# Performance work log

Hardware: AMD Instinct MI355X
Metric: run time of the kernel (lower is better)

## Reference

```python
import jax, jax.numpy as jnp
import numpy as np

B, N, R = 4, 16, 64        # batch, permuted axis size, inner spatial size
M, S = N // 2, R * 2       # block count, block size


def _glorot(key, shape):
    fan_in, fan_out = shape[-2], shape[-1]
    lim = np.sqrt(6.0 / (fan_in + fan_out)).astype(np.float32)
    return jax.random.uniform(key, shape, jnp.float32, -lim, lim)


def setup_inputs() -> dict:
    key = jax.random.key(0)
    ks = jax.random.split(key, 10)
    inp = {
        "x": jax.random.normal(ks[0], (B, N, R, N, R, 2), jnp.float32),
        "perm_idx": jax.random.permutation(ks[1], N).astype(jnp.int32),
    }
    for i, name in enumerate(["hr1", "hi1", "hr2", "hi2", "hr3", "hi3", "hr4", "hi4"]):
        inp[name] = _glorot(ks[2 + i], (M, S, S))
    return inp


def _bilin(v, p_right, p_left):
    # v: (B, m, s, m, s). First contract the last s-axis against p_right's
    # block matmuls (block index = axis 3), then the axis-2 s-axis against
    # p_left's block matmuls (block index = axis 1).
    t = jnp.einsum('bmiaj,ajk->bmiak', v, p_right)
    return jnp.einsum('xbjci,bjk->xbkci', t, p_left)


def reference(x, perm_idx, hr1, hi1, hr2, hi2, hr3, hi3, hr4, hi4):
    m = x.shape[1] // 2
    s = x.shape[2] * 2
    n, r = m * 2, s // 2
    x = x.take(perm_idx, axis=1).take(perm_idx, axis=3)
    x = x.reshape((-1, m, s, m, s, 2))
    x_re, x_im = x[..., 0], x[..., 1]

    y_re = (_bilin(x_re, hr1, hr1) + _bilin(x_re, hi1, hi1)
            + _bilin(x_im, hi2, hr2) + _bilin(x_im, hr2, hi2))
    y_im = (_bilin(x_im, hr3, hr3) + _bilin(x_im, hi3, hi3)
            + _bilin(x_re, hi4, hr4) + _bilin(x_re, hr4, hi4))

    y = jnp.stack([y_re, y_im], axis=-1)
    return y.reshape((-1, n, r, n, r, 2))
```

## Files before the change

kernel.cpp:

```cpp
#include <hip/hip_runtime.h>
#include <hip/hip_bf16.h>
#include <stdint.h>

typedef __attribute__((ext_vector_type(8))) short bf16x8;
typedef __attribute__((ext_vector_type(4))) float f32x4;
typedef __attribute__((ext_vector_type(16))) float f32x16;

#define MFMA32(a, b, c) __builtin_amdgcn_mfma_f32_32x32x16_bf16((a), (b), (c), 0, 0, 0)

__device__ __forceinline__ unsigned short f2bf_rn(float f) {
    union { __bf16 b; unsigned short u; } v;
    v.b = (__bf16)f;
    return v.u;
}

__device__ __forceinline__ unsigned int pk2(float lo, float hi) {
    union { unsigned short s[2]; unsigned int u; } r;
    r.s[0] = f2bf_rn(lo); r.s[1] = f2bf_rn(hi);
    return r.u;
}

__device__ __forceinline__ void gload_lds16(const void* g, void* l) {
    __builtin_amdgcn_global_load_lds(
        (const __attribute__((address_space(1))) void*)g,
        (__attribute__((address_space(3))) void*)l, 16, 0, 0);
}

__global__ __launch_bounds__(256) void prep_h(
    const float* __restrict__ h0, const float* __restrict__ h1,
    const float* __restrict__ h2, const float* __restrict__ h3,
    const float* __restrict__ h4, const float* __restrict__ h5,
    const float* __restrict__ h6, const float* __restrict__ h7,
    unsigned short* __restrict__ ht)
{
    const float* hmap[8] = {h0, h1, h2, h3, h4, h5, h6, h7};
    const int wg = blockIdx.x;
    const int jblk = wg >> 2, qt = wg & 3;
    const float* src = hmap[jblk >> 3] + (jblk & 7) * 16384;
    unsigned short* dst = ht + jblk * 16384;
    __shared__ unsigned short tile[32 * 129];
    const int t = threadIdx.x;
    #pragma unroll
    for (int i = 0; i < 16; ++i) {
        int idx = t + 256 * i;
        int r = idx >> 5, kk = idx & 31;
        tile[kk * 129 + r] = f2bf_rn(src[r * 128 + qt * 32 + kk]);
    }
    __syncthreads();
    #pragma unroll
    for (int i = 0; i < 16; ++i) {
        int idx = t + 256 * i;
        int k = idx >> 7, r = idx & 127;
        dst[(qt * 32 + k) * 128 + r] = tile[k * 129 + r];
    }
}

__global__ __launch_bounds__(256, 1) void bilin_main(
    const float* __restrict__ x, const int* __restrict__ perm,
    const unsigned short* __restrict__ ht, float* __restrict__ out)
{
    const int wg = blockIdx.x;
    const int q = wg & 7, p = (wg >> 3) & 7, b = wg >> 6;
    const int tid = threadIdx.x;
    const int lane = tid & 63, wn = tid >> 6;
    const int l31 = lane & 31, hl = lane >> 5;

    __shared__ __align__(16) unsigned short smem[81920];
    unsigned short* xre_lds = smem;
    unsigned short* xim_lds = smem + 16384;
    unsigned short* llds = smem + 65536;

    constexpr int cseq[8]  = {0, 1, 6, 7, 2, 3, 4, 5};
    constexpr int rperm[8] = {0, 1, 3, 2, 4, 5, 7, 6};

    const int wubase = tid & ~63;
    auto stage_h = [&](unsigned short* dst, int blk) {
        const unsigned short* src = ht + blk * 16384;
        #pragma unroll
        for (int r = 0; r < 8; ++r) {
            const int idx = r * 256 + tid;
            const int row = idx >> 4, cin = idx & 15;
            gload_lds16(src + row * 128 + ((cin ^ (row & 15)) << 3),
                        dst + ((r * 256 + wubase) << 3));
        }
    };

    auto ldr = [&](const unsigned short* base, int row, int ch) -> bf16x8 {
        return *(const bf16x8*)(base + row * 128 + ((ch ^ (row & 15)) << 3));
    };

    auto stage_x_both = [&]() {
        #pragma unroll
        for (int i = 0; i < 8; ++i) {
            const int idx = i * 256 + tid;
            const int row = idx >> 4, cin = idx & 15;
            const int n1 = perm[2 * p + (row >> 6)];
            const int n2 = perm[2 * q + (cin >> 3)];
            const int r1 = row & 63, r2 = (cin & 7) * 8;
            const float* sp = x + ((size_t)((b * 16 + n1) * 64 + r1) * 1024
                                   + n2 * 64 + r2) * 2;
            float4 v0 = *(const float4*)(sp);
            float4 v1 = *(const float4*)(sp + 4);
            float4 v2 = *(const float4*)(sp + 8);
            float4 v3 = *(const float4*)(sp + 12);
            bf16x8 re, im;
            re[0] = (short)f2bf_rn(v0.x); re[1] = (short)f2bf_rn(v0.z);
            re[2] = (short)f2bf_rn(v1.x); re[3] = (short)f2bf_rn(v1.z);
            re[4] = (short)f2bf_rn(v2.x); re[5] = (short)f2bf_rn(v2.z);
            re[6] = (short)f2bf_rn(v3.x); re[7] = (short)f2bf_rn(v3.z);
            im[0] = (short)f2bf_rn(v0.y); im[1] = (short)f2bf_rn(v0.w);
            im[2] = (short)f2bf_rn(v1.y); im[3] = (short)f2bf_rn(v1.w);
            im[4] = (short)f2bf_rn(v2.y); im[5] = (short)f2bf_rn(v2.w);
            im[6] = (short)f2bf_rn(v3.y); im[7] = (short)f2bf_rn(v3.w);
            const int woff = row * 128 + ((cin ^ (row & 15)) << 3);
            *(bf16x8*)(xre_lds + woff) = re;
            *(bf16x8*)(xim_lds + woff) = im;
        }
    };

    bf16x8 xf[4][8];
    auto load_xf = [&](const unsigned short* plane) {
        #pragma unroll
        for (int m2 = 0; m2 < 4; ++m2)
            #pragma unroll
            for (int ks = 0; ks < 8; ++ks)
                xf[m2][ks] = ldr(plane, m2 * 32 + l31, 2 * ks + hl);
    };

    stage_h(smem + 32768, rperm[0] * 8 + q);
    stage_h(llds, 0 * 8 + p);
    stage_x_both();
    __syncthreads();
    load_xf(xre_lds);

    f32x16 yre[4], yim[4];
    #pragma unroll
    for (int i = 0; i < 4; ++i) {
        #pragma unroll
        for (int e = 0; e < 16; ++e) { yre[i][e] = 0.f; yim[i][e] = 0.f; }
    }

    #pragma unroll
    for (int cc = 0; cc < 8; ++cc) {
        const unsigned short* wb = smem + 32768 + (cc & 1) * 16384;

        if (cc < 7)
            stage_h(smem + 32768 + ((cc + 1) & 1) * 16384,
                    rperm[cseq[cc + 1]] * 8 + q);

        if (cc == 4) load_xf(xim_lds);

        bf16x8 wfr[8];
        #pragma unroll
        for (int ks = 0; ks < 8; ++ks)
            wfr[ks] = ldr(wb, wn * 32 + l31, 2 * ks + hl);
        f32x16 u[4];
        #pragma unroll
        for (int m2 = 0; m2 < 4; ++m2)
            #pragma unroll
            for (int e = 0; e < 16; ++e) u[m2][e] = 0.f;
        #pragma unroll
        for (int ks = 0; ks < 8; ++ks)
            #pragma unroll
            for (int m2 = 0; m2 < 4; ++m2)
                u[m2] = MFMA32(xf[m2][ks], wfr[ks], u[m2]);

        __syncthreads();

        union UF { unsigned int d[4]; bf16x8 v; };
        UF ufu[8];
        #pragma unroll
        for (int t = 0; t < 8; ++t) {
            const int f = t >> 1, qa = (t & 1) * 2, qb = qa + 1;
            unsigned int lo0 = pk2(u[f][4 * qa + 0], u[f][4 * qa + 1]);
            unsigned int lo1 = pk2(u[f][4 * qa + 2], u[f][4 * qa + 3]);
            unsigned int hi0 = pk2(u[f][4 * qb + 0], u[f][4 * qb + 1]);
            unsigned int hi1 = pk2(u[f][4 * qb + 2], u[f][4 * qb + 3]);
            unsigned int send0 = hl ? lo0 : hi0;
            unsigned int send1 = hl ? lo1 : hi1;
            unsigned int sx0 = (unsigned int)__shfl_xor((int)send0, 32);
            unsigned int sx1 = (unsigned int)__shfl_xor((int)send1, 32);
            ufu[t].d[0] = hl ? sx0 : lo0;
            ufu[t].d[1] = hl ? sx1 : lo1;
            ufu[t].d[2] = hl ? hi0 : sx0;
            ufu[t].d[3] = hl ? hi1 : sx1;
        }
        const bool isRe = (cc & 3) < 2;
        bf16x8 lcur[4], lnxt[4];
        #pragma unroll
        for (int mt = 0; mt < 4; ++mt)
            lcur[mt] = ldr(llds, mt * 32 + l31, hl);
        #pragma unroll
        for (int t = 0; t < 8; ++t) {
            if (t < 7) {
                #pragma unroll
                for (int mt = 0; mt < 4; ++mt)
                    lnxt[mt] = ldr(llds, mt * 32 + l31, 2 * (t + 1) + hl);
            }
            #pragma unroll
            for (int mt = 0; mt < 4; ++mt) {
                if (isRe) yre[mt] = MFMA32(lcur[mt], ufu[t].v, yre[mt]);
                else      yim[mt] = MFMA32(lcur[mt], ufu[t].v, yim[mt]);
            }
            #pragma unroll
            for (int mt = 0; mt < 4; ++mt) lcur[mt] = lnxt[mt];
        }

        __syncthreads();
        if (cc < 7)
            stage_h(llds, cseq[cc + 1] * 8 + p);
    }

    float2* o2 = (float2*)out;
    #pragma unroll
    for (int mt = 0; mt < 4; ++mt)
        #pragma unroll
        for (int j = 0; j < 16; ++j) {
            const int row = mt * 32 + (j & 3) + 8 * (j >> 2) + 4 * hl;
            float2 v;
            v.x = yre[mt][j];
            v.y = yim[mt][j];
            o2[(size_t)(b * 1024 + p * 128 + row) * 1024
               + q * 128 + wn * 32 + l31] = v;
        }
}

extern "C" void kernel_launch(void* const* d_in, const int* in_sizes, int n_in,
                              void* d_out, int out_size, void* d_ws, size_t ws_size,
                              hipStream_t stream) {
    const float* x  = (const float*)d_in[0];
    const int* perm = (const int*)d_in[1];
    unsigned short* htp = (unsigned short*)d_ws;

    hipLaunchKernelGGL(prep_h, dim3(256), dim3(256), 0, stream,
        (const float*)d_in[2], (const float*)d_in[3], (const float*)d_in[4],
        (const float*)d_in[5], (const float*)d_in[6], (const float*)d_in[7],
        (const float*)d_in[8], (const float*)d_in[9], htp);
    hipLaunchKernelGGL(bilin_main, dim3(256), dim3(256), 0, stream,
        x, perm, htp, (float*)d_out);
}
```

Baseline: 38.19 us.

## Process real and imaginary chunks per phase; spill x imaginary plane to workspace

The eight sequential chunk iterations become four phases. Each phase computes one real-output and one imaginary-output chunk, using separate LDS buffers for the re/im right and left weight blocks, which halves the number of barrier-separated stages. To free LDS for the extra weight buffers, the imaginary x plane is written to a per-workgroup global workspace and copied back into LDS with global_load_lds while phase 0 runs. This adds global traffic and relies on the workspace being large enough and on writes from other threads in the block being visible after a barrier.

```diff
diff --git a/kernel.cpp b/kernel.cpp
--- a/kernel.cpp
+++ b/kernel.cpp
@@ -57,7 +57,9 @@
 
 __global__ __launch_bounds__(256, 1) void bilin_main(
     const float* __restrict__ x, const int* __restrict__ perm,
-    const unsigned short* __restrict__ ht, float* __restrict__ out)
+    const unsigned short* __restrict__ ht,
+    unsigned short* __restrict__ ximws,
+    float* __restrict__ out)
 {
     const int wg = blockIdx.x;
     const int q = wg & 7, p = (wg >> 3) & 7, b = wg >> 6;
@@ -66,11 +68,14 @@
     const int l31 = lane & 31, hl = lane >> 5;
 
     __shared__ __align__(16) unsigned short smem[81920];
-    unsigned short* xre_lds = smem;
-    unsigned short* xim_lds = smem + 16384;
-    unsigned short* llds = smem + 65536;
-
-    constexpr int cseq[8]  = {0, 1, 6, 7, 2, 3, 4, 5};
+    unsigned short* xplane = smem;
+    unsigned short* wre = smem + 16384;
+    unsigned short* wim = smem + 32768;
+    unsigned short* lre = smem + 49152;
+    unsigned short* lim = smem + 65536;
+
+    constexpr int pre_[4]  = {0, 1, 2, 3};
+    constexpr int pim_[4]  = {6, 7, 4, 5};
     constexpr int rperm[8] = {0, 1, 3, 2, 4, 5, 7, 6};
 
     const int wubase = tid & ~63;
@@ -88,6 +93,8 @@
     auto ldr = [&](const unsigned short* base, int row, int ch) -> bf16x8 {
         return *(const bf16x8*)(base + row * 128 + ((ch ^ (row & 15)) << 3));
     };
+
+    unsigned short* myxim = ximws + (size_t)wg * 16384;
 
     auto stage_x_both = [&]() {
         #pragma unroll
@@ -113,48 +120,34 @@
             im[4] = (short)f2bf_rn(v2.y); im[5] = (short)f2bf_rn(v2.w);
             im[6] = (short)f2bf_rn(v3.y); im[7] = (short)f2bf_rn(v3.w);
             const int woff = row * 128 + ((cin ^ (row & 15)) << 3);
-            *(bf16x8*)(xre_lds + woff) = re;
-            *(bf16x8*)(xim_lds + woff) = im;
+            *(bf16x8*)(xplane + woff) = re;
+            *(bf16x8*)(myxim + woff) = im;
+        }
+    };
+
+    auto restage_xim = [&]() {
+        #pragma unroll
+        for (int r = 0; r < 8; ++r) {
+            const int idx = r * 256 + tid;
+            gload_lds16(myxim + ((size_t)idx << 3),
+                        xplane + ((r * 256 + wubase) << 3));
         }
     };
 
     bf16x8 xf[4][8];
-    auto load_xf = [&](const unsigned short* plane) {
+    auto load_xf = [&]() {
         #pragma unroll
         for (int m2 = 0; m2 < 4; ++m2)
             #pragma unroll
             for (int ks = 0; ks < 8; ++ks)
-                xf[m2][ks] = ldr(plane, m2 * 32 + l31, 2 * ks + hl);
-    };
-
-    stage_h(smem + 32768, rperm[0] * 8 + q);
-    stage_h(llds, 0 * 8 + p);
-    stage_x_both();
-    __syncthreads();
-    load_xf(xre_lds);
-
-    f32x16 yre[4], yim[4];
-    #pragma unroll
-    for (int i = 0; i < 4; ++i) {
-        #pragma unroll
-        for (int e = 0; e < 16; ++e) { yre[i][e] = 0.f; yim[i][e] = 0.f; }
-    }
-
-    #pragma unroll
-    for (int cc = 0; cc < 8; ++cc) {
-        const unsigned short* wb = smem + 32768 + (cc & 1) * 16384;
-
-        if (cc < 7)
-            stage_h(smem + 32768 + ((cc + 1) & 1) * 16384,
-                    rperm[cseq[cc + 1]] * 8 + q);
-
-        if (cc == 4) load_xf(xim_lds);
-
+                xf[m2][ks] = ldr(xplane, m2 * 32 + l31, 2 * ks + hl);
+    };
+
+    auto do_A = [&](const unsigned short* wb, f32x16 (&u)[4]) {
         bf16x8 wfr[8];
         #pragma unroll
         for (int ks = 0; ks < 8; ++ks)
             wfr[ks] = ldr(wb, wn * 32 + l31, 2 * ks + hl);
-        f32x16 u[4];
         #pragma unroll
         for (int m2 = 0; m2 < 4; ++m2)
             #pragma unroll
@@ -164,9 +157,10 @@
             #pragma unroll
             for (int m2 = 0; m2 < 4; ++m2)
                 u[m2] = MFMA32(xf[m2][ks], wfr[ks], u[m2]);
-
-        __syncthreads();
-
+    };
+
+    auto do_B = [&](const f32x16 (&u)[4], const unsigned short* lb,
+                    f32x16 (&y)[4]) {
         union UF { unsigned int d[4]; bf16x8 v; };
         UF ufu[8];
         #pragma unroll
@@ -185,30 +179,61 @@
             ufu[t].d[2] = hl ? hi0 : sx0;
             ufu[t].d[3] = hl ? hi1 : sx1;
         }
-        const bool isRe = (cc & 3) < 2;
         bf16x8 lcur[4], lnxt[4];
         #pragma unroll
         for (int mt = 0; mt < 4; ++mt)
-            lcur[mt] = ldr(llds, mt * 32 + l31, hl);
+            lcur[mt] = ldr(lb, mt * 32 + l31, hl);
         #pragma unroll
         for (int t = 0; t < 8; ++t) {
             if (t < 7) {
                 #pragma unroll
                 for (int mt = 0; mt < 4; ++mt)
-                    lnxt[mt] = ldr(llds, mt * 32 + l31, 2 * (t + 1) + hl);
+                    lnxt[mt] = ldr(lb, mt * 32 + l31, 2 * (t + 1) + hl);
             }
             #pragma unroll
-            for (int mt = 0; mt < 4; ++mt) {
-                if (isRe) yre[mt] = MFMA32(lcur[mt], ufu[t].v, yre[mt]);
-                else      yim[mt] = MFMA32(lcur[mt], ufu[t].v, yim[mt]);
-            }
+            for (int mt = 0; mt < 4; ++mt)
+                y[mt] = MFMA32(lcur[mt], ufu[t].v, y[mt]);
             #pragma unroll
             for (int mt = 0; mt < 4; ++mt) lcur[mt] = lnxt[mt];
         }
+    };
+
+    stage_h(wre, rperm[pre_[0]] * 8 + q);
+    stage_h(wim, rperm[pim_[0]] * 8 + q);
+    stage_h(lre, pre_[0] * 8 + p);
+    stage_h(lim, pim_[0] * 8 + p);
+    stage_x_both();
+    __syncthreads();
+    load_xf();
+
+    f32x16 yre[4], yim[4], u[4];
+    #pragma unroll
+    for (int i = 0; i < 4; ++i)
+        #pragma unroll
+        for (int e = 0; e < 16; ++e) { yre[i][e] = 0.f; yim[i][e] = 0.f; }
+
+    #pragma unroll
+    for (int ph = 0; ph < 4; ++ph) {
+        do_A(wre, u);
 
         __syncthreads();
-        if (cc < 7)
-            stage_h(llds, cseq[cc + 1] * 8 + p);
+        if (ph < 3)
+            stage_h(wre, rperm[pre_[ph + 1]] * 8 + q);
+        if (ph == 0)
+            restage_xim();
+
+        do_B(u, lre, yre);
+        do_A(wim, u);
+        do_B(u, lim, yim);
+
+        __syncthreads();
+        if (ph < 3) {
+            stage_h(wim, rperm[pim_[ph + 1]] * 8 + q);
+            stage_h(lre, pre_[ph + 1] * 8 + p);
+            stage_h(lim, pim_[ph + 1] * 8 + p);
+        }
+        if (ph == 1)
+            load_xf();
     }
 
     float2* o2 = (float2*)out;
@@ -230,12 +255,14 @@
                               hipStream_t stream) {
     const float* x  = (const float*)d_in[0];
     const int* perm = (const int*)d_in[1];
-    unsigned short* htp = (unsigned short*)d_ws;
+    unsigned short* ws = (unsigned short*)d_ws;
+    unsigned short* htp   = ws;
+    unsigned short* ximws = ws + 1024u * 1024u;
 
     hipLaunchKernelGGL(prep_h, dim3(256), dim3(256), 0, stream,
         (const float*)d_in[2], (const float*)d_in[3], (const float*)d_in[4],
         (const float*)d_in[5], (const float*)d_in[6], (const float*)d_in[7],
         (const float*)d_in[8], (const float*)d_in[9], htp);
     hipLaunchKernelGGL(bilin_main, dim3(256), dim3(256), 0, stream,
-        x, perm, htp, (float*)d_out);
-}
+        x, perm, htp, ximws, (float*)d_out);
+}
```

Result: slower. 42.21 us (+10.5%).
